# Kernel optimization log

Measured on AMD Instinct MI355X. Metric: run time of the kernel, lower is better.

Reference implementation:

```python
import jax, jax.numpy as jnp
import numpy as np

MAX_BIN = 256
N_SAMPLES = 1_000_000
N_FEATURES = 100


def setup_inputs() -> dict:
    key = jax.random.key(0)
    k1, k2, k3 = jax.random.split(key, 3)
    X = jax.random.randint(k1, (N_SAMPLES, N_FEATURES), 0, MAX_BIN, dtype=jnp.int32)
    gradient = jax.random.normal(k2, (N_SAMPLES,), dtype=jnp.float32)
    hessian = jax.random.uniform(k3, (N_SAMPLES,), dtype=jnp.float32)
    return {"X": X, "gradient": gradient, "hessian": hessian}


def _histogram_cumsum(X, values, max_bin):
    # X: [N, F] int bins; values: [N] float.
    # hist[f, b] = sum_i values[i] * (X[i, f] == b); Gl[f, b] = sum_i values[i] * (X[i, f] <= b)
    n, f = X.shape
    # Combined segment id so a single segment_sum builds all per-feature histograms.
    seg = (X + jnp.arange(f, dtype=X.dtype)[None, :] * max_bin).reshape(-1)  # [N*F]
    vals = jnp.broadcast_to(values[:, None], (n, f)).reshape(-1)  # [N*F]
    hist = jax.ops.segment_sum(vals, seg, num_segments=f * max_bin)  # [F*max_bin]
    hist = hist.reshape(f, max_bin)
    return jnp.cumsum(hist, axis=1)  # left-sum per candidate split bin


def reference(X, gradient, hessian):
    Gl = _histogram_cumsum(X, gradient, MAX_BIN)  # [F, max_bin]
    Hl = _histogram_cumsum(X, hessian, MAX_BIN)   # [F, max_bin]
    return (Gl[None, :, :], Hl[None, :, :])
```

## Files before the change

### kernel.cpp

```cpp
#include <hip/hip_runtime.h>


#define F     100
#define FG    20
#define NG    5
#define BINS  256
#define TPB   1024
#define RPI   (TPB / 5)
#define CCHUNKS 102
#define SCALE_F 1048576.0f
#define INV_SCALE (1.0 / 1048576.0)

__global__ __launch_bounds__(512) void zero_kernel(unsigned long long* __restrict__ p)
{
    int i = blockIdx.x * 512 + threadIdx.x;
    if (i < 2 * F * BINS) p[i] = 0ULL;
}

__global__ __launch_bounds__(TPB) void hist_part_kernel(
    const int* __restrict__ X, const float* __restrict__ grad,
    const float* __restrict__ hess, unsigned long long* __restrict__ acc,
    int N, int rows_per_chunk)
{
    __shared__ unsigned long long hist[FG * BINS];
    const int tid  = threadIdx.x;
    const int c    = blockIdx.x / NG;
    const int grp  = blockIdx.x % NG;
    const int col0 = grp * FG;

    for (int i = tid; i < FG * BINS; i += TPB) hist[i] = 0ULL;
    __syncthreads();

    int r0 = c * rows_per_chunk;
    int r1 = r0 + rows_per_chunk;
    if (r1 > N) r1 = N;

    const int s = tid % 5;
    const int q = tid / 5;

    if (q < RPI) {
        const int fb = (4 * s) * BINS;
        const char* xb = (const char*)(X + col0 + 4 * s);

        int r = r0 + q;
        if (r < r1) {
            int4 cur = *(const int4*)(xb + (size_t)r * (F * 4));
            int  gq  = __float2int_rn(grad[r] * SCALE_F);
            int  hq  = __float2int_rn(hess[r] * SCALE_F);
            unsigned long long vc =
                ((unsigned long long)(unsigned int)gq << 32) | (unsigned int)hq;
            for (int rn = r + RPI; rn < r1; rn += RPI) {
                int4 nxt = *(const int4*)(xb + (size_t)rn * (F * 4));
                int  gn  = __float2int_rn(grad[rn] * SCALE_F);
                int  hn  = __float2int_rn(hess[rn] * SCALE_F);
                unsigned long long vn =
                    ((unsigned long long)(unsigned int)gn << 32) | (unsigned int)hn;
                atomicAdd(&hist[fb + 0 * BINS + cur.x], vc);
                atomicAdd(&hist[fb + 1 * BINS + cur.y], vc);
                atomicAdd(&hist[fb + 2 * BINS + cur.z], vc);
                atomicAdd(&hist[fb + 3 * BINS + cur.w], vc);
                cur = nxt; vc = vn;
            }
            atomicAdd(&hist[fb + 0 * BINS + cur.x], vc);
            atomicAdd(&hist[fb + 1 * BINS + cur.y], vc);
            atomicAdd(&hist[fb + 2 * BINS + cur.z], vc);
            atomicAdd(&hist[fb + 3 * BINS + cur.w], vc);
        }
    }
    __syncthreads();

    unsigned long long* g64 = acc;
    unsigned long long* h64 = acc + (size_t)F * BINS;
    for (int i = tid; i < FG * BINS; i += TPB) {
        unsigned long long v = hist[i];
        long long gi = (long long)(int)(v >> 32);
        unsigned long long hi = (unsigned long long)(unsigned int)v;
        atomicAdd(&g64[col0 * BINS + i], (unsigned long long)gi);
        atomicAdd(&h64[col0 * BINS + i], hi);
    }
}

__global__ __launch_bounds__(BINS) void scan_kernel(
    const unsigned long long* __restrict__ acc, float* __restrict__ out)
{
    __shared__ float sv[BINS];
    const int b = threadIdx.x;
    const int f = blockIdx.x % F;
    const int w = blockIdx.x / F;

    unsigned long long v = acc[(size_t)w * F * BINS + (size_t)f * BINS + b];
    sv[b] = (float)((double)(long long)v * INV_SCALE);
    __syncthreads();
#pragma unroll
    for (int off = 1; off < BINS; off <<= 1) {
        float t = (b >= off) ? sv[b - off] : 0.0f;
        __syncthreads();
        sv[b] += t;
        __syncthreads();
    }
    out[((size_t)w * F + f) * BINS + b] = sv[b];
}

extern "C" void kernel_launch(void* const* d_in, const int* in_sizes, int n_in,
                              void* d_out, int out_size, void* d_ws, size_t ws_size,
                              hipStream_t stream)
{
    const int*   X = (const int*)d_in[0];
    const float* g = (const float*)d_in[1];
    const float* h = (const float*)d_in[2];
    float*              out = (float*)d_out;
    unsigned long long* acc = (unsigned long long*)d_ws;
    const int N = in_sizes[1];

    const int C   = CCHUNKS;
    const int rpc = (N + C - 1) / C;

    hipLaunchKernelGGL(zero_kernel, dim3((2 * F * BINS + 511) / 512), dim3(512),
                       0, stream, acc);
    hipLaunchKernelGGL(hist_part_kernel, dim3(NG * C), dim3(TPB), 0, stream,
                       X, g, h, acc, N, rpc);
    hipLaunchKernelGGL(scan_kernel, dim3(2 * F), dim3(BINS), 0, stream,
                       acc, out);
}
```

Before: 569.6 us.

## Replace global atomic accumulation with per-chunk partials reduced in scan kernel

Each histogram block now writes its packed shared-memory histogram straight to a per-chunk partial buffer instead of doing 64-bit global atomics. The scan kernel sums the 102 partials per feature and bin, then scans gradient and hessian together. This removes the zero kernel and global atomic contention. In exchange it adds about 20 MB of partial writes and reads, and the final reduction runs on only 100 blocks.

```diff
diff --git a/kernel.cpp b/kernel.cpp
--- a/kernel.cpp
+++ b/kernel.cpp
@@ -11,15 +11,9 @@
 #define SCALE_F 1048576.0f
 #define INV_SCALE (1.0 / 1048576.0)
 
-__global__ __launch_bounds__(512) void zero_kernel(unsigned long long* __restrict__ p)
-{
-    int i = blockIdx.x * 512 + threadIdx.x;
-    if (i < 2 * F * BINS) p[i] = 0ULL;
-}
-
 __global__ __launch_bounds__(TPB) void hist_part_kernel(
     const int* __restrict__ X, const float* __restrict__ grad,
-    const float* __restrict__ hess, unsigned long long* __restrict__ acc,
+    const float* __restrict__ hess, unsigned long long* __restrict__ part,
     int N, int rows_per_chunk)
 {
     __shared__ unsigned long long hist[FG * BINS];
@@ -69,36 +63,41 @@
     }
     __syncthreads();
 
-    unsigned long long* g64 = acc;
-    unsigned long long* h64 = acc + (size_t)F * BINS;
-    for (int i = tid; i < FG * BINS; i += TPB) {
-        unsigned long long v = hist[i];
-        long long gi = (long long)(int)(v >> 32);
-        unsigned long long hi = (unsigned long long)(unsigned int)v;
-        atomicAdd(&g64[col0 * BINS + i], (unsigned long long)gi);
-        atomicAdd(&h64[col0 * BINS + i], hi);
-    }
+    unsigned long long* dst = part + (size_t)c * (F * BINS) + (size_t)col0 * BINS;
+    for (int i = tid; i < FG * BINS; i += TPB) dst[i] = hist[i];
 }
 
-__global__ __launch_bounds__(BINS) void scan_kernel(
-    const unsigned long long* __restrict__ acc, float* __restrict__ out)
+__global__ __launch_bounds__(BINS) void reduce_scan_kernel(
+    const unsigned long long* __restrict__ part, float* __restrict__ out)
 {
-    __shared__ float sv[BINS];
+    __shared__ float sg[BINS];
+    __shared__ float sh[BINS];
     const int b = threadIdx.x;
-    const int f = blockIdx.x % F;
-    const int w = blockIdx.x / F;
+    const int f = blockIdx.x;
 
-    unsigned long long v = acc[(size_t)w * F * BINS + (size_t)f * BINS + b];
-    sv[b] = (float)((double)(long long)v * INV_SCALE);
+    long long          gs = 0;
+    unsigned long long hs = 0;
+    const unsigned long long* p = part + (size_t)f * BINS + b;
+#pragma unroll 4
+    for (int c = 0; c < CCHUNKS; ++c) {
+        unsigned long long v = p[(size_t)c * (F * BINS)];
+        gs += (long long)(int)(v >> 32);
+        hs += (unsigned long long)(unsigned int)v;
+    }
+    sg[b] = (float)((double)gs * INV_SCALE);
+    sh[b] = (float)((double)hs * INV_SCALE);
     __syncthreads();
 #pragma unroll
     for (int off = 1; off < BINS; off <<= 1) {
-        float t = (b >= off) ? sv[b - off] : 0.0f;
+        float tg = (b >= off) ? sg[b - off] : 0.0f;
+        float th = (b >= off) ? sh[b - off] : 0.0f;
         __syncthreads();
-        sv[b] += t;
+        sg[b] += tg;
+        sh[b] += th;
         __syncthreads();
     }
-    out[((size_t)w * F + f) * BINS + b] = sv[b];
+    out[(size_t)f * BINS + b]             = sg[b];
+    out[(size_t)(F + f) * BINS + b]       = sh[b];
 }
 
 extern "C" void kernel_launch(void* const* d_in, const int* in_sizes, int n_in,
@@ -108,17 +107,15 @@
     const int*   X = (const int*)d_in[0];
     const float* g = (const float*)d_in[1];
     const float* h = (const float*)d_in[2];
-    float*              out = (float*)d_out;
-    unsigned long long* acc = (unsigned long long*)d_ws;
+    float*              out  = (float*)d_out;
+    unsigned long long* part = (unsigned long long*)d_ws;
     const int N = in_sizes[1];
 
     const int C   = CCHUNKS;
     const int rpc = (N + C - 1) / C;
 
-    hipLaunchKernelGGL(zero_kernel, dim3((2 * F * BINS + 511) / 512), dim3(512),
-                       0, stream, acc);
     hipLaunchKernelGGL(hist_part_kernel, dim3(NG * C), dim3(TPB), 0, stream,
-                       X, g, h, acc, N, rpc);
-    hipLaunchKernelGGL(scan_kernel, dim3(2 * F), dim3(BINS), 0, stream,
-                       acc, out);
+                       X, g, h, part, N, rpc);
+    hipLaunchKernelGGL(reduce_scan_kernel, dim3(F), dim3(BINS), 0, stream,
+                       part, out);
 }
```

After: 566.3 us. Within noise of the previous version (-0.6%).
